# Performance work log

Measured on AMD Instinct MI355X. Metric: run time of the kernel, lower is better.

## Reference

```python
import jax, jax.numpy as jnp
import numpy as np

D_MODEL = 1024
N_HEADS = 16
HEAD_DIM = D_MODEL // N_HEADS


def setup_inputs() -> dict:
    key = jax.random.key(0)
    ks = jax.random.split(key, 5)
    s = 0.02  # small init scale to keep softmax numerics reasonable
    x = jax.random.normal(ks[0], (4, 2048, D_MODEL), dtype=jnp.float32)
    w_qkv = jax.random.normal(ks[1], (D_MODEL, 3 * D_MODEL), dtype=jnp.float32) * s
    b_qkv = jnp.zeros((3 * D_MODEL,), dtype=jnp.float32)
    w_proj = jax.random.normal(ks[2], (D_MODEL, D_MODEL), dtype=jnp.float32) * s
    b_proj = jnp.zeros((D_MODEL,), dtype=jnp.float32)
    return {"x": x, "w_qkv": w_qkv, "b_qkv": b_qkv, "w_proj": w_proj, "b_proj": b_proj}


def reference(x, w_qkv, b_qkv, w_proj, b_proj):
    B, T, C = x.shape
    scale = 1.0 / np.sqrt(HEAD_DIM)
    qkv = x @ w_qkv + b_qkv                               # [B,T,3C]
    qkv = qkv.reshape(B, T, 3, N_HEADS, HEAD_DIM)
    q = qkv[:, :, 0].transpose(0, 2, 1, 3)               # [B,H,T,D]
    k = qkv[:, :, 1].transpose(0, 2, 1, 3)
    v = qkv[:, :, 2].transpose(0, 2, 1, 3)
    att = jnp.einsum('bhqd,bhkd->bhqk', q, k) * scale    # [B,H,T,T]
    causal = jnp.tril(jnp.ones((T, T), dtype=bool))
    att = jnp.where(causal, att, -jnp.inf)
    att = jax.nn.softmax(att, axis=-1)
    y = jnp.einsum('bhqk,bhkd->bhqd', att, v)            # [B,H,T,D]
    y = y.transpose(0, 2, 1, 3).reshape(B, T, C)
    y = y @ w_proj + b_proj
    return y
```

## Files before the change

### kernel.cpp

```cpp
#include <hip/hip_runtime.h>
#include <stdint.h>

#define BATCH 4
#define SEQ 2048
#define DMODEL 1024
#define NHEADS 16
#define HDIM 64
#define MROWS (BATCH * SEQ)

typedef float floatx4 __attribute__((ext_vector_type(4)));
typedef __bf16 bf16x8 __attribute__((ext_vector_type(8)));
typedef __bf16 bf16x4 __attribute__((ext_vector_type(4)));
typedef short short8 __attribute__((ext_vector_type(8)));

__device__ __forceinline__ unsigned short f32_to_bf16(float f) {
    union { float f; unsigned int u; } c; c.f = f;
    unsigned int u = c.u;
    unsigned int r = (u + 0x7FFFu + ((u >> 16) & 1u)) >> 16;
    return (unsigned short)r;
}

__device__ __forceinline__ void async_ld16(const void* g, void* l) {
    __builtin_amdgcn_global_load_lds(
        (const __attribute__((address_space(1))) unsigned int*)g,
        (__attribute__((address_space(3))) unsigned int*)l, 16, 0, 0);
}

#define BARRIER() do { asm volatile("" ::: "memory"); \
    __builtin_amdgcn_s_barrier(); asm volatile("" ::: "memory"); } while (0)

__global__ __launch_bounds__(256) void conv_f32_bf16(
    const float* __restrict__ in, unsigned short* __restrict__ out, int n4) {
    int i = blockIdx.x * 256 + threadIdx.x;
    if (i < n4) {
        float4 v = ((const float4*)in)[i];
        ushort4 o;
        o.x = f32_to_bf16(v.x); o.y = f32_to_bf16(v.y);
        o.z = f32_to_bf16(v.z); o.w = f32_to_bf16(v.w);
        ((ushort4*)out)[i] = o;
    }
}

__global__ __launch_bounds__(256) void transp_conv(
    const float* __restrict__ in, unsigned short* __restrict__ out, int K, int N) {
    __shared__ float tile[32][33];
    int bx = blockIdx.x * 32;
    int by = blockIdx.y * 32;
    int tx = threadIdx.x, ty = threadIdx.y;
#pragma unroll
    for (int i = 0; i < 4; ++i)
        tile[ty + i * 8][tx] = in[(size_t)(by + ty + i * 8) * N + bx + tx];
    __syncthreads();
#pragma unroll
    for (int i = 0; i < 4; ++i)
        out[(size_t)(bx + ty + i * 8) * K + by + tx] = f32_to_bf16(tile[tx][ty + i * 8]);
}

__global__ __launch_bounds__(256) void transp_bf16_head(
    const unsigned short* __restrict__ in, unsigned short* __restrict__ out) {
    __shared__ unsigned short tile[32][33];
    const unsigned short* src = in + (size_t)blockIdx.z * SEQ * HDIM;
    unsigned short* dst = out + (size_t)blockIdx.z * SEQ * HDIM;
    int bx = blockIdx.x * 32;
    int by = blockIdx.y * 32;
    int tx = threadIdx.x, ty = threadIdx.y;
#pragma unroll
    for (int i = 0; i < 4; ++i)
        tile[ty + i * 8][tx] = src[(size_t)(by + ty + i * 8) * HDIM + bx + tx];
    __syncthreads();
#pragma unroll
    for (int i = 0; i < 4; ++i) {
        int keyg = by + tx;
        int col2 = (keyg & ~63) | (((keyg & 15) << 2) | ((keyg >> 4) & 3));
        dst[(size_t)(bx + ty + i * 8) * SEQ + col2] = tile[tx][ty + i * 8];
    }
}

template <int EPI>
__global__ __launch_bounds__(512, 1) void gemm256(
    const unsigned short* __restrict__ A, const unsigned short* __restrict__ Bt,
    const float* __restrict__ bias, float* __restrict__ Cout,
    unsigned short* __restrict__ Qo, unsigned short* __restrict__ Ko,
    unsigned short* __restrict__ Vo, int M, int N, int K) {
    __shared__ __align__(16) unsigned short ldsA[2][2][8192];
    __shared__ __align__(16) unsigned short ldsB[2][2][8192];

    const int tid = threadIdx.x;
    const int lane = tid & 63;
    const int w = tid >> 6;
    const int wm = w >> 2, wn = w & 3;
    const int quad = lane >> 4, l16 = lane & 15;
    const int m0 = blockIdx.y * 256;
    const int n0 = blockIdx.x * 256;
    const int ldb = K * 2;
    const int NT = K >> 6;

    const int t16 = tid * 16;
    const int soff = t16 ^ (((t16 >> 9) & 1) << 5);
    const int srow = soff >> 7;
    const int scol = soff & 127;
    const char* pAs = (const char*)A + (size_t)(m0 + srow) * ldb + scol;
    const char* pBs = (const char*)Bt + (size_t)(n0 + srow) * ldb + scol;
    char* ldA0 = (char*)&ldsA[0][0][0] + t16;
    char* ldB0 = (char*)&ldsB[0][0][0] + t16;

    auto stA = [&](int kt, int uu) {
        async_ld16(pAs + (size_t)uu * 64 * ldb + kt * 128,
                   ldA0 + ((kt & 1) << 15) + (uu << 13));
    };
    auto stB = [&](int kt, int uu) {
        async_ld16(pBs + (size_t)uu * 64 * ldb + kt * 128,
                   ldB0 + ((kt & 1) << 15) + (uu << 13));
    };

    const int xle = ((l16 >> 2) & 1) << 4;

    floatx4 acc[8][4];
#pragma unroll
    for (int mf = 0; mf < 8; ++mf)
#pragma unroll
        for (int nf = 0; nf < 4; ++nf) acc[mf][nf] = (floatx4){0.f, 0.f, 0.f, 0.f};

    stA(0, 0); stA(0, 1); stA(0, 2); stA(0, 3);
    stB(0, 0); stB(0, 1); stB(0, 2); stB(0, 3);
    if (NT > 1) {
        stA(1, 0); stA(1, 2);
        stB(1, 0); stB(1, 2);
        stA(1, 1); stA(1, 3);
    }

#define MFMA16(dst, af, bf) dst = __builtin_amdgcn_mfma_f32_16x16x32_bf16(af, bf, dst, 0, 0, 0)

    for (int t = 0; t < NT; ++t) {
        const int b = t & 1;
        if (t + 1 < NT) asm volatile("s_waitcnt vmcnt(6)" ::: "memory");
        else            asm volatile("s_waitcnt vmcnt(0)" ::: "memory");
        BARRIER();

        const unsigned short* Ab = &ldsA[b][wm][0];
        const unsigned short* Bb = &ldsB[b][wn >> 1][(wn & 1) * 4096];

        bf16x8 aR[4][2], bR[4][2];

#pragma unroll
        for (int mf = 0; mf < 4; ++mf)
#pragma unroll
            for (int kk = 0; kk < 2; ++kk)
                aR[mf][kk] = *(const bf16x8*)&Ab[(mf * 16 + l16) * 64 +
                                                 ((kk * 32 + quad * 8) ^ xle)];
#pragma unroll
        for (int nf = 0; nf < 2; ++nf)
#pragma unroll
            for (int kk = 0; kk < 2; ++kk)
                bR[nf][kk] = *(const bf16x8*)&Bb[(nf * 16 + l16) * 64 +
                                                 ((kk * 32 + quad * 8) ^ xle)];
        if (t + 1 < NT) { stB(t + 1, 1); stB(t + 1, 3); }
        BARRIER();
        __builtin_amdgcn_s_setprio(1);
#pragma unroll
        for (int mf = 0; mf < 4; ++mf)
#pragma unroll
            for (int nf = 0; nf < 2; ++nf)
#pragma unroll
                for (int kk = 0; kk < 2; ++kk)
                    MFMA16(acc[mf][nf], aR[mf][kk], bR[nf][kk]);
        __builtin_amdgcn_s_setprio(0);
        BARRIER();

#pragma unroll
        for (int nf = 2; nf < 4; ++nf)
#pragma unroll
            for (int kk = 0; kk < 2; ++kk)
                bR[nf][kk] = *(const bf16x8*)&Bb[(nf * 16 + l16) * 64 +
                                                 ((kk * 32 + quad * 8) ^ xle)];
        if (t + 2 < NT) { stA(t + 2, 0); stA(t + 2, 2); }
        BARRIER();
        __builtin_amdgcn_s_setprio(1);
#pragma unroll
        for (int mf = 0; mf < 4; ++mf)
#pragma unroll
            for (int nf = 2; nf < 4; ++nf)
#pragma unroll
                for (int kk = 0; kk < 2; ++kk)
                    MFMA16(acc[mf][nf], aR[mf][kk], bR[nf][kk]);
        __builtin_amdgcn_s_setprio(0);
        BARRIER();

#pragma unroll
        for (int mf = 0; mf < 4; ++mf)
#pragma unroll
            for (int kk = 0; kk < 2; ++kk)
                aR[mf][kk] = *(const bf16x8*)&Ab[((mf + 4) * 16 + l16) * 64 +
                                                 ((kk * 32 + quad * 8) ^ xle)];
        if (t + 2 < NT) { stB(t + 2, 0); stB(t + 2, 2); }
        BARRIER();
        __builtin_amdgcn_s_setprio(1);
#pragma unroll
        for (int mf = 0; mf < 4; ++mf)
#pragma unroll
            for (int nf = 2; nf < 4; ++nf)
#pragma unroll
                for (int kk = 0; kk < 2; ++kk)
                    MFMA16(acc[mf + 4][nf], aR[mf][kk], bR[nf][kk]);
        __builtin_amdgcn_s_setprio(0);
        BARRIER();

        if (t + 2 < NT) { stA(t + 2, 1); stA(t + 2, 3); }
        BARRIER();
        __builtin_amdgcn_s_setprio(1);
#pragma unroll
        for (int mf = 0; mf < 4; ++mf)
#pragma unroll
            for (int nf = 0; nf < 2; ++nf)
#pragma unroll
                for (int kk = 0; kk < 2; ++kk)
                    MFMA16(acc[mf + 4][nf], aR[mf][kk], bR[nf][kk]);
        __builtin_amdgcn_s_setprio(0);
    }
#undef MFMA16

#pragma unroll
    for (int mf = 0; mf < 8; ++mf)
#pragma unroll
        for (int nf = 0; nf < 4; ++nf)
#pragma unroll
            for (int r = 0; r < 4; ++r) {
                int m = m0 + wm * 128 + mf * 16 + quad * 4 + r;
                int n = n0 + wn * 64 + nf * 16 + l16;
                float v = acc[mf][nf][r] + bias[n];
                if (EPI == 1) {
                    Cout[(size_t)m * N + n] = v;
                } else {
                    int sel = n >> 10, c = n & 1023;
                    int head = c >> 6, d = c & 63;
                    int bb = m >> 11, tt = m & 2047;
                    unsigned short* dst = sel == 0 ? Qo : (sel == 1 ? Ko : Vo);
                    dst[((((size_t)bb * NHEADS + head) * SEQ + tt) << 6) + d] = f32_to_bf16(v);
                }
            }
}

__global__ __launch_bounds__(256, 2) void attn_kernel(
    const unsigned short* __restrict__ Qg, const unsigned short* __restrict__ Kg,
    const unsigned short* __restrict__ Vtg, unsigned short* __restrict__ Yatt) {
    __shared__ __align__(16) unsigned short Kb2[2][4096];
    __shared__ __align__(16) unsigned short Vb2[2][4096];
    __shared__ __align__(16) unsigned short Ps[4][2048];

    const int tid = threadIdx.x;
    const int lane = tid & 63;
    const int w = tid >> 6;
    const int quad = lane >> 4, l16 = lane & 15;
    const int bh = blockIdx.x;
    const int by = blockIdx.y;
    const int sA = by * 4 + w;
    const size_t base = (size_t)bh * SEQ * HDIM;
    const int bIdx = bh >> 4, h = bh & 15;
    unsigned short* Pw = &Ps[w][0];
    const float csc = 0.18033688f;

    const int lrow = lane >> 3;
    const int lch = (lane & 7) ^ lrow;

    short8 osv = {0x3F80, 0x3F80, 0x3F80, 0x3F80, 0x3F80, 0x3F80, 0x3F80, 0x3F80};
    bf16x8 ones = __builtin_bit_cast(bf16x8, osv);

    for (int half = 0; half < 2; ++half) {
        const int rowb = (half == 0 ? sA : 63 - sA) * 32;
        const int kmaxB = (half == 0) ? (2 * by + 2) : (32 - 2 * by);

        bf16x8 qf[2][2];
#pragma unroll
        for (int mt = 0; mt < 2; ++mt)
#pragma unroll
            for (int kk = 0; kk < 2; ++kk)
                qf[mt][kk] = *(const bf16x8*)&Qg[base + (size_t)(rowb + mt * 16 + l16) * 64 +
                                                 kk * 32 + quad * 8];

        floatx4 lsum[2];
        floatx4 o[2][4];
#pragma unroll
        for (int mt = 0; mt < 2; ++mt) {
            lsum[mt] = (floatx4){0.f, 0.f, 0.f, 0.f};
#pragma unroll
            for (int nt = 0; nt < 4; ++nt) o[mt][nt] = (floatx4){0.f, 0.f, 0.f, 0.f};
        }

        {
            const unsigned short* Ktg = Kg + base;
            const unsigned short* Vtg_t = Vtg + base;
#pragma unroll
            for (int ii = 0; ii < 2; ++ii) {
                int i = w * 2 + ii;
                async_ld16(Ktg + (i * 8 + lrow) * 64 + lch * 8,
                           &Kb2[0][i * 512 + lane * 8]);
                async_ld16(Vtg_t + (size_t)(i * 8 + lrow) * SEQ + lch * 8,
                           &Vb2[0][i * 512 + lane * 8]);
            }
        }

        for (int kb = 0; kb < kmaxB; ++kb) {
            const int b = kb & 1;
            __syncthreads();

            if (kb + 1 < kmaxB) {
                const unsigned short* Ktg = Kg + base + (size_t)(kb + 1) * 64 * HDIM;
                const unsigned short* Vtg_t = Vtg + base + (kb + 1) * 64;
#pragma unroll
                for (int ii = 0; ii < 2; ++ii) {
                    int i = w * 2 + ii;
                    async_ld16(Ktg + (i * 8 + lrow) * 64 + lch * 8,
                               &Kb2[1 - b][i * 512 + lane * 8]);
                    async_ld16(Vtg_t + (size_t)(i * 8 + lrow) * SEQ + lch * 8,
                               &Vb2[1 - b][i * 512 + lane * 8]);
                }
            }

            floatx4 s[2][4];
#pragma unroll
            for (int mt = 0; mt < 2; ++mt)
#pragma unroll
                for (int nt = 0; nt < 4; ++nt) s[mt][nt] = (floatx4){0.f, 0.f, 0.f, 0.f};
#pragma unroll
            for (int kk = 0; kk < 2; ++kk) {
                bf16x8 kf[4];
#pragma unroll
                for (int nt = 0; nt < 4; ++nt)
                    kf[nt] = *(const bf16x8*)&Kb2[b][(nt * 16 + l16) * 64 +
                                                     ((kk * 4 + quad) ^ (l16 & 7)) * 8];
#pragma unroll
                for (int nt = 0; nt < 4; ++nt)
#pragma unroll
                    for (int mt = 0; mt < 2; ++mt)
                        s[mt][nt] = __builtin_amdgcn_mfma_f32_16x16x32_bf16(
                            qf[mt][kk], kf[nt], s[mt][nt], 0, 0, 0);
            }

            if ((kb * 64 + 63) > rowb) {
#pragma unroll
                for (int mt = 0; mt < 2; ++mt)
#pragma unroll
                    for (int nt = 0; nt < 4; ++nt)
#pragma unroll
                        for (int r = 0; r < 4; ++r) {
                            int key = kb * 64 + nt * 16 + l16;
                            int qrow = rowb + mt * 16 + quad * 4 + r;
                            if (key > qrow) s[mt][nt][r] = -INFINITY;
                        }
            }

#pragma unroll
            for (int mt = 0; mt < 2; ++mt)
#pragma unroll
                for (int nt = 0; nt < 4; ++nt)
#pragma unroll
                    for (int r = 0; r < 4; ++r)
                        s[mt][nt][r] = __builtin_amdgcn_exp2f(s[mt][nt][r] * csc);

#pragma unroll
            for (int mt = 0; mt < 2; ++mt)
#pragma unroll
                for (int r = 0; r < 4; ++r) {
                    int prow = mt * 16 + quad * 4 + r;
                    int unit = l16 ^ (prow & 14);
                    floatx4 t = {s[mt][0][r], s[mt][1][r], s[mt][2][r], s[mt][3][r]};
                    bf16x4 pv = __builtin_convertvector(t, bf16x4);
                    *(bf16x4*)&Pw[prow * 64 + unit * 4] = pv;
                }

#pragma unroll
            for (int kk = 0; kk < 2; ++kk) {
                bf16x8 af[2];
#pragma unroll
                for (int mt = 0; mt < 2; ++mt) {
                    int prow = mt * 16 + l16;
                    int u2 = (kk * 8 + quad * 2) ^ (l16 & 14);
                    af[mt] = *(const bf16x8*)&Pw[prow * 64 + u2 * 4];
                }
#pragma unroll
                for (int nt = 0; nt < 4; ++nt) {
                    bf16x8 vf = *(const bf16x8*)&Vb2[b][(nt * 16 + l16) * 64 +
                                                        ((kk * 4 + quad) ^ (l16 & 7)) * 8];
#pragma unroll
                    for (int mt = 0; mt < 2; ++mt)
                        o[mt][nt] = __builtin_amdgcn_mfma_f32_16x16x32_bf16(
                            af[mt], vf, o[mt][nt], 0, 0, 0);
                }
#pragma unroll
                for (int mt = 0; mt < 2; ++mt)
                    lsum[mt] = __builtin_amdgcn_mfma_f32_16x16x32_bf16(
                        af[mt], ones, lsum[mt], 0, 0, 0);
            }
        }

#pragma unroll
        for (int mt = 0; mt < 2; ++mt)
#pragma unroll
            for (int r = 0; r < 4; ++r) {
                float inv = 1.0f / lsum[mt][r];
                int qrow = rowb + mt * 16 + quad * 4 + r;
#pragma unroll
                for (int nt = 0; nt < 4; ++nt)
                    Yatt[((size_t)(bIdx * SEQ + qrow) << 10) + h * 64 + nt * 16 + l16] =
                        f32_to_bf16(o[mt][nt][r] * inv);
            }
    }
}

extern "C" void kernel_launch(void* const* d_in, const int* in_sizes, int n_in,
                              void* d_out, int out_size, void* d_ws, size_t ws_size,
                              hipStream_t stream) {
    const float* x = (const float*)d_in[0];
    const float* w_qkv = (const float*)d_in[1];
    const float* b_qkv = (const float*)d_in[2];
    const float* w_proj = (const float*)d_in[3];
    const float* b_proj = (const float*)d_in[4];
    float* out = (float*)d_out;

    char* ws = (char*)d_ws;
    unsigned short* xb     = (unsigned short*)(ws);
    unsigned short* wqkvT  = (unsigned short*)(ws + 16777216);
    unsigned short* wprojT = (unsigned short*)(ws + 23068672);
    unsigned short* Qb     = (unsigned short*)(ws + 25165824);
    unsigned short* Kb     = (unsigned short*)(ws + 41943040);
    unsigned short* Vb     = (unsigned short*)(ws + 58720256);
    unsigned short* Yatt   = (unsigned short*)(ws + 75497472);
    unsigned short* Vt     = (unsigned short*)(ws + 92274688);

    conv_f32_bf16<<<8192, 256, 0, stream>>>(x, xb, (MROWS * DMODEL) / 4);
    transp_conv<<<dim3(96, 32), dim3(32, 8), 0, stream>>>(w_qkv, wqkvT, DMODEL, 3 * DMODEL);
    transp_conv<<<dim3(32, 32), dim3(32, 8), 0, stream>>>(w_proj, wprojT, DMODEL, DMODEL);
    gemm256<0><<<dim3(12, 32), 512, 0, stream>>>(xb, wqkvT, b_qkv, nullptr, Qb, Kb, Vb,
                                                 MROWS, 3 * DMODEL, DMODEL);
    transp_bf16_head<<<dim3(2, 64, BATCH * NHEADS), dim3(32, 8), 0, stream>>>(Vb, Vt);
    attn_kernel<<<dim3(64, 8), 256, 0, stream>>>(Qb, Kb, Vt, Yatt);
    gemm256<1><<<dim3(4, 32), 512, 0, stream>>>(Yatt, wprojT, b_proj, out, nullptr, nullptr,
                                                nullptr, MROWS, DMODEL, DMODEL);
}
```

Before: 276.3 us.

## Use 128x128 triple-buffered GEMM for projection and 8-way LDS swizzle

Changes the gemm256 LDS layout to an XOR swizzle over eight 16-byte slots per row, applied both on the async global-to-LDS writes and on the fragment reads, to reduce LDS bank conflicts. It also adds a smaller gemm_bt kernel with 128x128 tiles, K-step 32 and triple-buffered async loads, and uses it for the output projection. That GEMM has N=1024, so the smaller tile gives 512 blocks instead of 128, which is meant to fill the CUs better. The cost is less data reuse per block and more barriers per unit of K.

```diff
diff --git a/kernel.cpp b/kernel.cpp
--- a/kernel.cpp
+++ b/kernel.cpp
@@ -96,11 +96,10 @@
     const int NT = K >> 6;
 
     const int t16 = tid * 16;
-    const int soff = t16 ^ (((t16 >> 9) & 1) << 5);
-    const int srow = soff >> 7;
-    const int scol = soff & 127;
-    const char* pAs = (const char*)A + (size_t)(m0 + srow) * ldb + scol;
-    const char* pBs = (const char*)Bt + (size_t)(n0 + srow) * ldb + scol;
+    const int srow = tid >> 3;
+    const int sslot = (tid & 7) ^ (srow & 7);
+    const char* pAs = (const char*)A + (size_t)(m0 + srow) * ldb + sslot * 16;
+    const char* pBs = (const char*)Bt + (size_t)(n0 + srow) * ldb + sslot * 16;
     char* ldA0 = (char*)&ldsA[0][0][0] + t16;
     char* ldB0 = (char*)&ldsB[0][0][0] + t16;
 
@@ -113,8 +112,6 @@
                    ldB0 + ((kt & 1) << 15) + (uu << 13));
     };
 
-    const int xle = ((l16 >> 2) & 1) << 4;
-
     floatx4 acc[8][4];
 #pragma unroll
     for (int mf = 0; mf < 8; ++mf)
@@ -130,6 +127,7 @@
     }
 
 #define MFMA16(dst, af, bf) dst = __builtin_amdgcn_mfma_f32_16x16x32_bf16(af, bf, dst, 0, 0, 0)
+#define RD(base, row, s) (*(const bf16x8*)&(base)[(row) * 64 + (((s) ^ ((row) & 7)) << 3)])
 
     for (int t = 0; t < NT; ++t) {
         const int b = t & 1;
@@ -146,14 +144,12 @@
         for (int mf = 0; mf < 4; ++mf)
 #pragma unroll
             for (int kk = 0; kk < 2; ++kk)
-                aR[mf][kk] = *(const bf16x8*)&Ab[(mf * 16 + l16) * 64 +
-                                                 ((kk * 32 + quad * 8) ^ xle)];
+                aR[mf][kk] = RD(Ab, mf * 16 + l16, kk * 4 + quad);
 #pragma unroll
         for (int nf = 0; nf < 2; ++nf)
 #pragma unroll
             for (int kk = 0; kk < 2; ++kk)
-                bR[nf][kk] = *(const bf16x8*)&Bb[(nf * 16 + l16) * 64 +
-                                                 ((kk * 32 + quad * 8) ^ xle)];
+                bR[nf][kk] = RD(Bb, nf * 16 + l16, kk * 4 + quad);
         if (t + 1 < NT) { stB(t + 1, 1); stB(t + 1, 3); }
         BARRIER();
         __builtin_amdgcn_s_setprio(1);
@@ -171,8 +167,7 @@
         for (int nf = 2; nf < 4; ++nf)
 #pragma unroll
             for (int kk = 0; kk < 2; ++kk)
-                bR[nf][kk] = *(const bf16x8*)&Bb[(nf * 16 + l16) * 64 +
-                                                 ((kk * 32 + quad * 8) ^ xle)];
+                bR[nf][kk] = RD(Bb, nf * 16 + l16, kk * 4 + quad);
         if (t + 2 < NT) { stA(t + 2, 0); stA(t + 2, 2); }
         BARRIER();
         __builtin_amdgcn_s_setprio(1);
@@ -190,8 +185,7 @@
         for (int mf = 0; mf < 4; ++mf)
 #pragma unroll
             for (int kk = 0; kk < 2; ++kk)
-                aR[mf][kk] = *(const bf16x8*)&Ab[((mf + 4) * 16 + l16) * 64 +
-                                                 ((kk * 32 + quad * 8) ^ xle)];
+                aR[mf][kk] = RD(Ab, (mf + 4) * 16 + l16, kk * 4 + quad);
         if (t + 2 < NT) { stB(t + 2, 0); stB(t + 2, 2); }
         BARRIER();
         __builtin_amdgcn_s_setprio(1);
@@ -217,6 +211,7 @@
                     MFMA16(acc[mf + 4][nf], aR[mf][kk], bR[nf][kk]);
         __builtin_amdgcn_s_setprio(0);
     }
+#undef RD
 #undef MFMA16
 
 #pragma unroll
@@ -240,6 +235,104 @@
             }
 }
 
+template <int EPI>
+__global__ __launch_bounds__(256, 3) void gemm_bt(
+    const unsigned short* __restrict__ A, const unsigned short* __restrict__ Bt,
+    const float* __restrict__ bias, float* __restrict__ Cout,
+    unsigned short* __restrict__ Qo, unsigned short* __restrict__ Ko,
+    unsigned short* __restrict__ Vo, int M, int N, int K) {
+    __shared__ __align__(16) unsigned short As[3][128 * 32];
+    __shared__ __align__(16) unsigned short Bs[3][128 * 32];
+    const int tid = threadIdx.x;
+    const int lane = tid & 63;
+    const int w = tid >> 6;
+    const int wm = w & 1, wn = w >> 1;
+    const int quad = lane >> 4, l16 = lane & 15;
+    const int m0 = blockIdx.y * 128;
+    const int n0 = blockIdx.x * 128;
+    const int fsw = (l16 >> 1) & 3;
+
+    const int idx0 = tid, idx1 = tid + 256;
+    const int row0 = idx0 >> 2, row1 = idx1 >> 2;
+    const int cg0 = (idx0 & 3) ^ ((row0 >> 1) & 3);
+    const int cg1 = (idx1 & 3) ^ ((row1 >> 1) & 3);
+    const unsigned short* Ar0 = &A[(size_t)(m0 + row0) * K + cg0 * 8];
+    const unsigned short* Ar1 = &A[(size_t)(m0 + row1) * K + cg1 * 8];
+    const unsigned short* Br0 = &Bt[(size_t)(n0 + row0) * K + cg0 * 8];
+    const unsigned short* Br1 = &Bt[(size_t)(n0 + row1) * K + cg1 * 8];
+
+    floatx4 acc[4][4];
+#pragma unroll
+    for (int mt = 0; mt < 4; ++mt)
+#pragma unroll
+        for (int nt = 0; nt < 4; ++nt) acc[mt][nt] = (floatx4){0.f, 0.f, 0.f, 0.f};
+
+    async_ld16(Ar0, &As[0][idx0 * 8]);
+    async_ld16(Br0, &Bs[0][idx0 * 8]);
+    async_ld16(Ar1, &As[0][idx1 * 8]);
+    async_ld16(Br1, &Bs[0][idx1 * 8]);
+    async_ld16(Ar0 + 32, &As[1][idx0 * 8]);
+    async_ld16(Br0 + 32, &Bs[1][idx0 * 8]);
+    async_ld16(Ar1 + 32, &As[1][idx1 * 8]);
+    async_ld16(Br1 + 32, &Bs[1][idx1 * 8]);
+
+    const int nk = K >> 5;
+    int bcur = 0, bpre = 2;
+    for (int kt = 0; kt < nk; ++kt) {
+        if (kt + 2 < nk)
+            asm volatile("s_waitcnt vmcnt(4)" ::: "memory");
+        else
+            asm volatile("s_waitcnt vmcnt(0)" ::: "memory");
+        __builtin_amdgcn_s_barrier();
+        asm volatile("" ::: "memory");
+
+        if (kt + 2 < nk) {
+            const int ko = (kt + 2) << 5;
+            async_ld16(Ar0 + ko, &As[bpre][idx0 * 8]);
+            async_ld16(Br0 + ko, &Bs[bpre][idx0 * 8]);
+            async_ld16(Ar1 + ko, &As[bpre][idx1 * 8]);
+            async_ld16(Br1 + ko, &Bs[bpre][idx1 * 8]);
+        }
+
+        bf16x8 aF[4], bF[4];
+#pragma unroll
+        for (int mt = 0; mt < 4; ++mt)
+            aF[mt] = *(const bf16x8*)&As[bcur][(wm * 64 + mt * 16 + l16) * 32 + (quad ^ fsw) * 8];
+#pragma unroll
+        for (int nt = 0; nt < 4; ++nt)
+            bF[nt] = *(const bf16x8*)&Bs[bcur][(wn * 64 + nt * 16 + l16) * 32 + (quad ^ fsw) * 8];
+#pragma unroll
+        for (int mt = 0; mt < 4; ++mt)
+#pragma unroll
+            for (int nt = 0; nt < 4; ++nt)
+                acc[mt][nt] = __builtin_amdgcn_mfma_f32_16x16x32_bf16(
+                    aF[mt], bF[nt], acc[mt][nt], 0, 0, 0);
+
+        bcur = (bcur == 2) ? 0 : bcur + 1;
+        bpre = (bpre == 2) ? 0 : bpre + 1;
+    }
+
+#pragma unroll
+    for (int mt = 0; mt < 4; ++mt)
+#pragma unroll
+        for (int nt = 0; nt < 4; ++nt)
+#pragma unroll
+            for (int r = 0; r < 4; ++r) {
+                int m = m0 + wm * 64 + mt * 16 + quad * 4 + r;
+                int n = n0 + wn * 64 + nt * 16 + l16;
+                float v = acc[mt][nt][r] + bias[n];
+                if (EPI == 1) {
+                    Cout[(size_t)m * N + n] = v;
+                } else {
+                    int sel = n >> 10, c = n & 1023;
+                    int head = c >> 6, d = c & 63;
+                    int bb = m >> 11, t = m & 2047;
+                    unsigned short* dst = sel == 0 ? Qo : (sel == 1 ? Ko : Vo);
+                    dst[((((size_t)bb * NHEADS + head) * SEQ + t) << 6) + d] = f32_to_bf16(v);
+                }
+            }
+}
+
 __global__ __launch_bounds__(256, 2) void attn_kernel(
     const unsigned short* __restrict__ Qg, const unsigned short* __restrict__ Kg,
     const unsigned short* __restrict__ Vtg, unsigned short* __restrict__ Yatt) {
@@ -434,6 +527,6 @@
                                                  MROWS, 3 * DMODEL, DMODEL);
     transp_bf16_head<<<dim3(2, 64, BATCH * NHEADS), dim3(32, 8), 0, stream>>>(Vb, Vt);
     attn_kernel<<<dim3(64, 8), 256, 0, stream>>>(Qb, Kb, Vt, Yatt);
-    gemm256<1><<<dim3(4, 32), 512, 0, stream>>>(Yatt, wprojT, b_proj, out, nullptr, nullptr,
+    gemm_bt<1><<<dim3(8, 64), 256, 0, stream>>>(Yatt, wprojT, b_proj, out, nullptr, nullptr,
                                                 nullptr, MROWS, DMODEL, DMODEL);
 }
```

New measurement: 261.7 us. -5.3%, faster.
